# Performance work log

Measured on AMD Instinct MI355X. Metric: run time of the kernel, lower is better.

## Reference

```python
import jax, jax.numpy as jnp
import numpy as np

N = 100000
E = 1600000
F_IN = 32
HID = 16


def _sage_conv(x, src, dst, W_l, b_l, W_r):
    # PyG SAGEConv (aggr='mean', normalize=False, root_weight=True):
    #   out = lin_l(mean_{j in N(i)} x_j) + lin_r(x_i)
    # lin_l has bias, lin_r has no bias.
    n = x.shape[0]
    msg_sum = jax.ops.segment_sum(x[src], dst, num_segments=n)          # [N, d]
    deg = jax.ops.segment_sum(jnp.ones_like(dst, dtype=x.dtype), dst, num_segments=n)
    agg = msg_sum / jnp.maximum(deg, 1.0)[:, None]                      # mean, 0 for isolated nodes
    return agg @ W_l.T + b_l + x @ W_r.T


def setup_inputs() -> dict:
    key = jax.random.key(0)
    ks = jax.random.split(key, 8)
    x = jax.random.normal(ks[0], (N, F_IN), dtype=jnp.float32)
    edge_index = jax.random.randint(ks[1], (1, 2, E), 0, N, dtype=jnp.int64)
    s1 = 1.0 / np.sqrt(F_IN)
    s2 = 1.0 / np.sqrt(HID)
    W1_l = jax.random.uniform(ks[2], (HID, F_IN), jnp.float32, -s1, s1)
    b1_l = jax.random.uniform(ks[3], (HID,), jnp.float32, -s1, s1)
    W1_r = jax.random.uniform(ks[4], (HID, F_IN), jnp.float32, -s1, s1)
    W2_l = jax.random.uniform(ks[5], (F_IN, HID), jnp.float32, -s2, s2)
    b2_l = jax.random.uniform(ks[6], (F_IN,), jnp.float32, -s2, s2)
    W2_r = jax.random.uniform(ks[7], (F_IN, HID), jnp.float32, -s2, s2)
    return {"x": x, "edge_index": edge_index, "W1_l": W1_l, "b1_l": b1_l,
            "W1_r": W1_r, "W2_l": W2_l, "b2_l": b2_l, "W2_r": W2_r}


def reference(x, edge_index, W1_l, b1_l, W1_r, W2_l, b2_l, W2_r):
    ei = jnp.squeeze(edge_index, axis=0)  # [2, E]
    src, dst = ei[0], ei[1]
    h = jax.nn.relu(_sage_conv(x, src, dst, W1_l, b1_l, W1_r))
    out = _sage_conv(h, src, dst, W2_l, b2_l, W2_r)
    return out
```

## Files before the change

kernel.cpp:

```cpp
#include <hip/hip_runtime.h>

#define F_IN 32
#define HID 16
#define BSHIFT 7
#define BNODES (1 << BSHIFT)
#define CAP 2560
#define CHUNK 8192
#define SRCM 0x1FFFFu
#define WS1 33
#define WS2 17

__device__ __forceinline__ void add4(float4& a, const float4& b) {
    a.x += b.x; a.y += b.y; a.z += b.z; a.w += b.w;
}
__device__ __forceinline__ unsigned pack2(float a, float b) {
    unsigned ua = __float_as_uint(a);
    unsigned ub = __float_as_uint(b);
    ua = (ua + 0x7FFFu + ((ua >> 16) & 1u)) >> 16;
    ub = (ub + 0x7FFFu + ((ub >> 16) & 1u)) >> 16;
    return ua | (ub << 16);
}
__device__ __forceinline__ float lo2f(unsigned u) { return __uint_as_float(u << 16); }
__device__ __forceinline__ float hi2f(unsigned u) { return __uint_as_float(u & 0xFFFF0000u); }
__device__ __forceinline__ float4 unp(uint2 v) {
    return make_float4(lo2f(v.x), hi2f(v.x), lo2f(v.y), hi2f(v.y));
}

__global__ void __launch_bounds__(256) k_pre(const float* __restrict__ x,
                                             const float* __restrict__ W1_l,
                                             unsigned* __restrict__ y1b,
                                             const int* __restrict__ ei,
                                             int* __restrict__ bucketCursor,
                                             unsigned* __restrict__ bucketBuf,
                                             int N, int E, int nodeBlocks) {
    __shared__ int cnt[1024];
    __shared__ int runBase[1024];
    __shared__ float Ws[HID * F_IN];
    int tid = threadIdx.x;

    if ((int)blockIdx.x < nodeBlocks) {
        for (int i = tid; i < HID * F_IN; i += 256) Ws[i] = W1_l[i];
        __syncthreads();
        int node = blockIdx.x * 256 + tid;
        if (node >= N) return;
        float xr[F_IN];
        const float4* xp = (const float4*)(x + (size_t)node * F_IN);
#pragma unroll
        for (int i = 0; i < F_IN / 4; i++) {
            float4 v = xp[i];
            xr[4 * i + 0] = v.x; xr[4 * i + 1] = v.y;
            xr[4 * i + 2] = v.z; xr[4 * i + 3] = v.w;
        }
        float a[HID];
#pragma unroll
        for (int o = 0; o < HID; o++) {
            float s = 0.f;
#pragma unroll
            for (int k = 0; k < F_IN; k++) s += xr[k] * Ws[o * F_IN + k];
            a[o] = s;
        }
        uint4* yp = (uint4*)(y1b + (size_t)node * 8);
        yp[0] = make_uint4(pack2(a[0], a[1]), pack2(a[2], a[3]),
                           pack2(a[4], a[5]), pack2(a[6], a[7]));
        yp[1] = make_uint4(pack2(a[8], a[9]), pack2(a[10], a[11]),
                           pack2(a[12], a[13]), pack2(a[14], a[15]));
        return;
    }

    int pb = blockIdx.x - nodeBlocks;
    int e0 = pb * CHUNK;
    int e1 = min(e0 + CHUNK, E);
    int n4 = (e1 - e0) >> 2;
    const int4* dst4 = (const int4*)(ei + E + e0);
    const int4* src4 = (const int4*)(ei + e0);

#pragma unroll
    for (int i = 0; i < 4; i++) cnt[tid + 256 * i] = 0;
    __syncthreads();
    for (int i = tid; i < n4; i += 256) {
        int4 d = dst4[i];
        atomicAdd(&cnt[d.x >> BSHIFT], 1);
        atomicAdd(&cnt[d.y >> BSHIFT], 1);
        atomicAdd(&cnt[d.z >> BSHIFT], 1);
        atomicAdd(&cnt[d.w >> BSHIFT], 1);
    }
    __syncthreads();
#pragma unroll
    for (int i = 0; i < 4; i++) {
        int b = tid + 256 * i;
        int c = cnt[b];
        runBase[b] = c ? atomicAdd(&bucketCursor[b], c) : 0;
        cnt[b] = 0;
    }
    __syncthreads();
    for (int i = tid; i < n4; i += 256) {
        int4 d = dst4[i];
        int4 s = src4[i];
        {
            int b = d.x >> BSHIFT;
            int pos = runBase[b] + atomicAdd(&cnt[b], 1);
            if (pos < CAP)
                bucketBuf[(size_t)b * CAP + pos] = ((unsigned)(d.x & (BNODES - 1)) << 17) | (unsigned)s.x;
        }
        {
            int b = d.y >> BSHIFT;
            int pos = runBase[b] + atomicAdd(&cnt[b], 1);
            if (pos < CAP)
                bucketBuf[(size_t)b * CAP + pos] = ((unsigned)(d.y & (BNODES - 1)) << 17) | (unsigned)s.y;
        }
        {
            int b = d.z >> BSHIFT;
            int pos = runBase[b] + atomicAdd(&cnt[b], 1);
            if (pos < CAP)
                bucketBuf[(size_t)b * CAP + pos] = ((unsigned)(d.z & (BNODES - 1)) << 17) | (unsigned)s.z;
        }
        {
            int b = d.w >> BSHIFT;
            int pos = runBase[b] + atomicAdd(&cnt[b], 1);
            if (pos < CAP)
                bucketBuf[(size_t)b * CAP + pos] = ((unsigned)(d.w & (BNODES - 1)) << 17) | (unsigned)s.w;
        }
    }
}

__global__ void __launch_bounds__(256) k_agg1f(const unsigned* __restrict__ y1b,
                                               const float* __restrict__ x,
                                               unsigned* __restrict__ bucketBuf,
                                               const int* __restrict__ bucketCursor,
                                               const float* __restrict__ W1_r,
                                               const float* __restrict__ b1,
                                               unsigned* __restrict__ hb,
                                               int* __restrict__ meta, int N) {
    __shared__ __align__(16) unsigned sA[CAP];
    __shared__ __align__(16) unsigned sB[CAP];
    __shared__ int hist[BNODES];
    __shared__ int scn[BNODES];
    __shared__ int cur[BNODES];
    __shared__ float Ws[HID * WS1];
    __shared__ float bs[HID];
    int tid = threadIdx.x, b = blockIdx.x;

    for (int i = tid; i < HID * F_IN; i += 256) Ws[(i >> 5) * WS1 + (i & 31)] = W1_r[i];
    if (tid < HID) bs[tid] = b1[tid];
    if (tid < BNODES) hist[tid] = 0;
    int nRec = min(bucketCursor[b], CAP);
    unsigned* buf = bucketBuf + (size_t)b * CAP;
    int n4s = (nRec + 3) >> 2;
    for (int i = tid; i < n4s; i += 256)
        ((uint4*)sA)[i] = ((const uint4*)buf)[i];
    __syncthreads();
    for (int i = tid; i < nRec; i += 256) atomicAdd(&hist[sA[i] >> 17], 1);
    __syncthreads();
    if (tid < BNODES) scn[tid] = hist[tid];
    __syncthreads();
    for (int off = 1; off < BNODES; off <<= 1) {
        int v = (tid < BNODES && tid >= off) ? scn[tid - off] : 0;
        __syncthreads();
        if (tid < BNODES && tid >= off) scn[tid] += v;
        __syncthreads();
    }
    if (tid < BNODES) cur[tid] = scn[tid] - hist[tid];
    __syncthreads();
    for (int i = tid; i < nRec; i += 256) {
        unsigned r = sA[i];
        int pos = atomicAdd(&cur[r >> 17], 1);
        sB[pos] = r & SRCM;
    }
    __syncthreads();

    for (int i = tid; i < n4s; i += 256)
        ((uint4*)buf)[i] = ((const uint4*)sB)[i];
    if (tid < BNODES) {
        meta[(size_t)b * 256 + tid] = scn[tid] - hist[tid];
        meta[(size_t)b * 256 + BNODES + tid] = scn[tid];
    }

    const uint2* yv = (const uint2*)y1b;
#pragma unroll
    for (int pass = 0; pass < 2; pass++) {
        int slot = pass * 256 + tid;
        int nl = slot >> 2, c = slot & 3;
        int node = b * BNODES + nl;
        if (node >= N) continue;
        int start = scn[nl] - hist[nl];
        int dg = hist[nl];
        int jend = start + dg;
        float4 a0 = make_float4(0, 0, 0, 0), a1 = a0;
        int j = start;
        for (; j + 4 <= jend; j += 4) {
            unsigned s0 = sB[j], s1 = sB[j + 1], s2 = sB[j + 2], s3 = sB[j + 3];
            uint2 v0 = yv[(size_t)s0 * 4 + c];
            uint2 v1 = yv[(size_t)s1 * 4 + c];
            uint2 v2 = yv[(size_t)s2 * 4 + c];
            uint2 v3 = yv[(size_t)s3 * 4 + c];
            add4(a0, unp(v0)); add4(a1, unp(v1));
            add4(a0, unp(v2)); add4(a1, unp(v3));
        }
        for (; j < jend; j++) {
            uint2 v = yv[(size_t)sB[j] * 4 + c];
            add4(a0, unp(v));
        }
        add4(a0, a1);
        float inv = 1.0f / (float)(dg > 0 ? dg : 1);
        float m[4] = {a0.x * inv, a0.y * inv, a0.z * inv, a0.w * inv};

        float xr[F_IN];
        const float4* xp = (const float4*)(x + (size_t)node * F_IN);
#pragma unroll
        for (int q = 0; q < F_IN / 4; q++) {
            float4 v = xp[q];
            xr[4 * q + 0] = v.x; xr[4 * q + 1] = v.y;
            xr[4 * q + 2] = v.z; xr[4 * q + 3] = v.w;
        }
        float a[4];
#pragma unroll
        for (int jj = 0; jj < 4; jj++) {
            int o = c * 4 + jj;
            float s = m[jj] + bs[o];
#pragma unroll
            for (int k = 0; k < F_IN; k++) s += xr[k] * Ws[o * WS1 + k];
            a[jj] = fmaxf(s, 0.0f);
        }
        ((uint2*)hb)[(size_t)node * 4 + c] = make_uint2(pack2(a[0], a[1]), pack2(a[2], a[3]));
    }
}

__global__ void __launch_bounds__(256) k_l2f(const unsigned* __restrict__ hb,
                                             const unsigned* __restrict__ bucketBuf,
                                             const int* __restrict__ bucketCursor,
                                             const int* __restrict__ meta,
                                             const float* __restrict__ W2_l,
                                             const float* __restrict__ b2,
                                             const float* __restrict__ W2_r,
                                             float* __restrict__ out, int N) {
    __shared__ __align__(16) unsigned sB[CAP];
    __shared__ int s0[BNODES];
    __shared__ int s1[BNODES];
    __shared__ float mm[BNODES * (HID + 1)];
    __shared__ float Wl[F_IN * WS2];
    __shared__ float Wr[F_IN * WS2];
    __shared__ float bs[F_IN];
    int tid = threadIdx.x, b = blockIdx.x;

    for (int i = tid; i < F_IN * HID; i += 256) {
        int r = i >> 4, q = i & 15;
        Wl[r * WS2 + q] = W2_l[i];
        Wr[r * WS2 + q] = W2_r[i];
    }
    if (tid < F_IN) bs[tid] = b2[tid];
    if (tid < BNODES) {
        s0[tid] = meta[(size_t)b * 256 + tid];
        s1[tid] = meta[(size_t)b * 256 + BNODES + tid];
    }
    int nRec = min(bucketCursor[b], CAP);
    const uint4* bv = (const uint4*)(bucketBuf + (size_t)b * CAP);
    int n4s = (nRec + 3) >> 2;
    for (int i = tid; i < n4s; i += 256) ((uint4*)sB)[i] = bv[i];
    __syncthreads();

    const uint2* hv = (const uint2*)hb;
#pragma unroll
    for (int pass = 0; pass < 2; pass++) {
        int slot = pass * 256 + tid;
        int nl = slot >> 2, c = slot & 3;
        int node = b * BNODES + nl;
        if (node >= N) continue;
        int start = s0[nl];
        int jend = s1[nl];
        int dg = jend - start;
        float4 a0 = make_float4(0, 0, 0, 0), a1 = a0;
        int j = start;
        for (; j + 4 <= jend; j += 4) {
            unsigned v0i = sB[j], v1i = sB[j + 1], v2i = sB[j + 2], v3i = sB[j + 3];
            uint2 v0 = hv[(size_t)v0i * 4 + c];
            uint2 v1 = hv[(size_t)v1i * 4 + c];
            uint2 v2 = hv[(size_t)v2i * 4 + c];
            uint2 v3 = hv[(size_t)v3i * 4 + c];
            add4(a0, unp(v0)); add4(a1, unp(v1));
            add4(a0, unp(v2)); add4(a1, unp(v3));
        }
        for (; j < jend; j++) {
            uint2 v = hv[(size_t)sB[j] * 4 + c];
            add4(a0, unp(v));
        }
        add4(a0, a1);
        float inv = 1.0f / (float)(dg > 0 ? dg : 1);
        mm[nl * (HID + 1) + c * 4 + 0] = a0.x * inv;
        mm[nl * (HID + 1) + c * 4 + 1] = a0.y * inv;
        mm[nl * (HID + 1) + c * 4 + 2] = a0.z * inv;
        mm[nl * (HID + 1) + c * 4 + 3] = a0.w * inv;
    }
    __syncthreads();

#pragma unroll
    for (int pass = 0; pass < 2; pass++) {
        int slot = pass * 256 + tid;
        int nl = slot >> 2, c = slot & 3;
        int node = b * BNODES + nl;
        if (node >= N) continue;

        float m[HID];
#pragma unroll
        for (int k = 0; k < HID; k++) m[k] = mm[nl * (HID + 1) + k];

        float hr[HID];
        const uint4* hp = (const uint4*)(hb + (size_t)node * 8);
        uint4 u0 = hp[0], u1 = hp[1];
        hr[0] = lo2f(u0.x); hr[1] = hi2f(u0.x); hr[2] = lo2f(u0.y); hr[3] = hi2f(u0.y);
        hr[4] = lo2f(u0.z); hr[5] = hi2f(u0.z); hr[6] = lo2f(u0.w); hr[7] = hi2f(u0.w);
        hr[8] = lo2f(u1.x); hr[9] = hi2f(u1.x); hr[10] = lo2f(u1.y); hr[11] = hi2f(u1.y);
        hr[12] = lo2f(u1.z); hr[13] = hi2f(u1.z); hr[14] = lo2f(u1.w); hr[15] = hi2f(u1.w);

        float a[8];
#pragma unroll
        for (int jj = 0; jj < 8; jj++) {
            int o = c * 8 + jj;
            float s = bs[o];
#pragma unroll
            for (int k = 0; k < HID; k++)
                s += m[k] * Wl[o * WS2 + k] + hr[k] * Wr[o * WS2 + k];
            a[jj] = s;
        }
        float4* op = (float4*)(out + (size_t)node * F_IN + c * 8);
        op[0] = make_float4(a[0], a[1], a[2], a[3]);
        op[1] = make_float4(a[4], a[5], a[6], a[7]);
    }
}

extern "C" void kernel_launch(void* const* d_in, const int* in_sizes, int n_in,
                              void* d_out, int out_size, void* d_ws, size_t ws_size,
                              hipStream_t stream) {
    const float* x    = (const float*)d_in[0];
    const int*   ei   = (const int*)d_in[1];
    const float* W1_l = (const float*)d_in[2];
    const float* b1   = (const float*)d_in[3];
    const float* W1_r = (const float*)d_in[4];
    const float* W2_l = (const float*)d_in[5];
    const float* b2   = (const float*)d_in[6];
    const float* W2_r = (const float*)d_in[7];
    float* out = (float*)d_out;

    const int N = in_sizes[0] / F_IN;
    const int E = in_sizes[1] / 2;
    const int nbuckets = (N + BNODES - 1) >> BSHIFT;

    int* bucketCursor = (int*)d_ws;
    unsigned* bucketBuf = (unsigned*)(bucketCursor + 1024);
    unsigned* y1b = bucketBuf + (size_t)nbuckets * CAP;
    unsigned* hb  = y1b + (size_t)N * 8;
    int* meta = (int*)(hb + (size_t)N * 8);

    hipMemsetAsync(bucketCursor, 0, 1024 * sizeof(int), stream);

    const int nodeBlocks = (N + 255) / 256;
    const int partBlocks = (E + CHUNK - 1) / CHUNK;

    k_pre<<<nodeBlocks + partBlocks, 256, 0, stream>>>(x, W1_l, y1b, ei,
                                                       bucketCursor, bucketBuf,
                                                       N, E, nodeBlocks);
    k_agg1f<<<nbuckets, 256, 0, stream>>>(y1b, x, bucketBuf, bucketCursor,
                                          W1_r, b1, hb, meta, N);
    k_l2f<<<nbuckets, 256, 0, stream>>>(hb, bucketBuf, bucketCursor, meta,
                                        W2_l, b2, W2_r, out, N);
}
```

Before: 152.0 us.

## Locally sort edge chunks in LDS and precompute root transform in pre-kernel

The edge partition blocks now counting-sort their chunk by bucket in shared memory first, then write each bucket's records to global memory as contiguous runs. This replaces the scattered per-edge global writes and is meant to improve write coalescing. The chunk size is halved so the sorted chunk fits in shared memory. The layer-1 root projection (x·W1_r plus bias) also moves into the node blocks of the pre-kernel and is stored as an fp32 buffer, so the aggregation kernel no longer rereads x or does the matmul. The cost is an extra 64 bytes per node of global traffic and more partition blocks with a scan step.

After: 172.8 us. 1.14x slower.

```diff
diff --git a/kernel.cpp b/kernel.cpp
--- a/kernel.cpp
+++ b/kernel.cpp
@@ -5,9 +5,9 @@
 #define BSHIFT 7
 #define BNODES (1 << BSHIFT)
 #define CAP 2560
-#define CHUNK 8192
+#define CHUNK 4096
+#define NBINS 1024
 #define SRCM 0x1FFFFu
-#define WS1 33
 #define WS2 17
 
 __device__ __forceinline__ void add4(float4& a, const float4& b) {
@@ -28,18 +28,23 @@
 
 __global__ void __launch_bounds__(256) k_pre(const float* __restrict__ x,
                                              const float* __restrict__ W1_l,
+                                             const float* __restrict__ b1,
+                                             const float* __restrict__ W1_r,
                                              unsigned* __restrict__ y1b,
+                                             float* __restrict__ y1r,
                                              const int* __restrict__ ei,
                                              int* __restrict__ bucketCursor,
                                              unsigned* __restrict__ bucketBuf,
                                              int N, int E, int nodeBlocks) {
-    __shared__ int cnt[1024];
-    __shared__ int runBase[1024];
-    __shared__ float Ws[HID * F_IN];
+    __shared__ __align__(16) unsigned char smem[37888];
     int tid = threadIdx.x;
 
     if ((int)blockIdx.x < nodeBlocks) {
-        for (int i = tid; i < HID * F_IN; i += 256) Ws[i] = W1_l[i];
+        float* Wa = (float*)smem;
+        float* Wb = (float*)(smem + 2048);
+        float* bb = (float*)(smem + 4096);
+        for (int i = tid; i < HID * F_IN; i += 256) { Wa[i] = W1_l[i]; Wb[i] = W1_r[i]; }
+        if (tid < HID) bb[tid] = b1[tid];
         __syncthreads();
         int node = blockIdx.x * 256 + tid;
         if (node >= N) return;
@@ -56,7 +61,7 @@
         for (int o = 0; o < HID; o++) {
             float s = 0.f;
 #pragma unroll
-            for (int k = 0; k < F_IN; k++) s += xr[k] * Ws[o * F_IN + k];
+            for (int k = 0; k < F_IN; k++) s += xr[k] * Wa[o * F_IN + k];
             a[o] = s;
         }
         uint4* yp = (uint4*)(y1b + (size_t)node * 8);
@@ -64,71 +69,108 @@
                            pack2(a[4], a[5]), pack2(a[6], a[7]));
         yp[1] = make_uint4(pack2(a[8], a[9]), pack2(a[10], a[11]),
                            pack2(a[12], a[13]), pack2(a[14], a[15]));
+#pragma unroll
+        for (int o = 0; o < HID; o++) {
+            float s = bb[o];
+#pragma unroll
+            for (int k = 0; k < F_IN; k++) s += xr[k] * Wb[o * F_IN + k];
+            a[o] = s;
+        }
+        float4* rp = (float4*)(y1r + (size_t)node * HID);
+        rp[0] = make_float4(a[0], a[1], a[2], a[3]);
+        rp[1] = make_float4(a[4], a[5], a[6], a[7]);
+        rp[2] = make_float4(a[8], a[9], a[10], a[11]);
+        rp[3] = make_float4(a[12], a[13], a[14], a[15]);
         return;
     }
+
+    unsigned* sRec = (unsigned*)smem;
+    unsigned short* sBkt = (unsigned short*)(smem + 16384);
+    int* hist    = (int*)(smem + 24576);
+    int* cur     = (int*)(smem + 28672);
+    int* runBase = (int*)(smem + 32768);
+    int* tmp     = (int*)(smem + 36864);
 
     int pb = blockIdx.x - nodeBlocks;
     int e0 = pb * CHUNK;
-    int e1 = min(e0 + CHUNK, E);
-    int n4 = (e1 - e0) >> 2;
+    int n = min(CHUNK, E - e0);
+    int n4 = n >> 2;
     const int4* dst4 = (const int4*)(ei + E + e0);
     const int4* src4 = (const int4*)(ei + e0);
 
 #pragma unroll
-    for (int i = 0; i < 4; i++) cnt[tid + 256 * i] = 0;
+    for (int i = 0; i < 4; i++) hist[tid + 256 * i] = 0;
     __syncthreads();
     for (int i = tid; i < n4; i += 256) {
         int4 d = dst4[i];
-        atomicAdd(&cnt[d.x >> BSHIFT], 1);
-        atomicAdd(&cnt[d.y >> BSHIFT], 1);
-        atomicAdd(&cnt[d.z >> BSHIFT], 1);
-        atomicAdd(&cnt[d.w >> BSHIFT], 1);
-    }
-    __syncthreads();
-#pragma unroll
-    for (int i = 0; i < 4; i++) {
-        int b = tid + 256 * i;
-        int c = cnt[b];
-        runBase[b] = c ? atomicAdd(&bucketCursor[b], c) : 0;
-        cnt[b] = 0;
-    }
+        atomicAdd(&hist[d.x >> BSHIFT], 1);
+        atomicAdd(&hist[d.y >> BSHIFT], 1);
+        atomicAdd(&hist[d.z >> BSHIFT], 1);
+        atomicAdd(&hist[d.w >> BSHIFT], 1);
+    }
+    __syncthreads();
+    int h0 = hist[4 * tid + 0], h1 = hist[4 * tid + 1];
+    int h2 = hist[4 * tid + 2], h3 = hist[4 * tid + 3];
+    int ssum = h0 + h1 + h2 + h3;
+    tmp[tid] = ssum;
+    __syncthreads();
+    for (int off = 1; off < 256; off <<= 1) {
+        int v = (tid >= off) ? tmp[tid - off] : 0;
+        __syncthreads();
+        if (tid >= off) tmp[tid] += v;
+        __syncthreads();
+    }
+    int excl = tmp[tid] - ssum;
+    cur[4 * tid + 0] = excl;
+    cur[4 * tid + 1] = excl + h0;
+    cur[4 * tid + 2] = excl + h0 + h1;
+    cur[4 * tid + 3] = excl + h0 + h1 + h2;
+    runBase[4 * tid + 0] = h0 ? atomicAdd(&bucketCursor[4 * tid + 0], h0) : 0;
+    runBase[4 * tid + 1] = h1 ? atomicAdd(&bucketCursor[4 * tid + 1], h1) : 0;
+    runBase[4 * tid + 2] = h2 ? atomicAdd(&bucketCursor[4 * tid + 2], h2) : 0;
+    runBase[4 * tid + 3] = h3 ? atomicAdd(&bucketCursor[4 * tid + 3], h3) : 0;
     __syncthreads();
     for (int i = tid; i < n4; i += 256) {
         int4 d = dst4[i];
         int4 s = src4[i];
         {
             int b = d.x >> BSHIFT;
-            int pos = runBase[b] + atomicAdd(&cnt[b], 1);
-            if (pos < CAP)
-                bucketBuf[(size_t)b * CAP + pos] = ((unsigned)(d.x & (BNODES - 1)) << 17) | (unsigned)s.x;
+            int pos = atomicAdd(&cur[b], 1);
+            sRec[pos] = ((unsigned)(d.x & (BNODES - 1)) << 17) | (unsigned)s.x;
+            sBkt[pos] = (unsigned short)b;
         }
         {
             int b = d.y >> BSHIFT;
-            int pos = runBase[b] + atomicAdd(&cnt[b], 1);
-            if (pos < CAP)
-                bucketBuf[(size_t)b * CAP + pos] = ((unsigned)(d.y & (BNODES - 1)) << 17) | (unsigned)s.y;
+            int pos = atomicAdd(&cur[b], 1);
+            sRec[pos] = ((unsigned)(d.y & (BNODES - 1)) << 17) | (unsigned)s.y;
+            sBkt[pos] = (unsigned short)b;
         }
         {
             int b = d.z >> BSHIFT;
-            int pos = runBase[b] + atomicAdd(&cnt[b], 1);
-            if (pos < CAP)
-                bucketBuf[(size_t)b * CAP + pos] = ((unsigned)(d.z & (BNODES - 1)) << 17) | (unsigned)s.z;
+            int pos = atomicAdd(&cur[b], 1);
+            sRec[pos] = ((unsigned)(d.z & (BNODES - 1)) << 17) | (unsigned)s.z;
+            sBkt[pos] = (unsigned short)b;
         }
         {
             int b = d.w >> BSHIFT;
-            int pos = runBase[b] + atomicAdd(&cnt[b], 1);
-            if (pos < CAP)
-                bucketBuf[(size_t)b * CAP + pos] = ((unsigned)(d.w & (BNODES - 1)) << 17) | (unsigned)s.w;
-        }
+            int pos = atomicAdd(&cur[b], 1);
+            sRec[pos] = ((unsigned)(d.w & (BNODES - 1)) << 17) | (unsigned)s.w;
+            sBkt[pos] = (unsigned short)b;
+        }
+    }
+    __syncthreads();
+    for (int p = tid; p < n; p += 256) {
+        int b = sBkt[p];
+        int start = cur[b] - hist[b];
+        int bpos = runBase[b] + (p - start);
+        if (bpos < CAP) bucketBuf[(size_t)b * CAP + bpos] = sRec[p];
     }
 }
 
 __global__ void __launch_bounds__(256) k_agg1f(const unsigned* __restrict__ y1b,
-                                               const float* __restrict__ x,
+                                               const float* __restrict__ y1r,
                                                unsigned* __restrict__ bucketBuf,
                                                const int* __restrict__ bucketCursor,
-                                               const float* __restrict__ W1_r,
-                                               const float* __restrict__ b1,
                                                unsigned* __restrict__ hb,
                                                int* __restrict__ meta, int N) {
     __shared__ __align__(16) unsigned sA[CAP];
@@ -136,12 +178,8 @@
     __shared__ int hist[BNODES];
     __shared__ int scn[BNODES];
     __shared__ int cur[BNODES];
-    __shared__ float Ws[HID * WS1];
-    __shared__ float bs[HID];
     int tid = threadIdx.x, b = blockIdx.x;
 
-    for (int i = tid; i < HID * F_IN; i += 256) Ws[(i >> 5) * WS1 + (i & 31)] = W1_r[i];
-    if (tid < HID) bs[tid] = b1[tid];
     if (tid < BNODES) hist[tid] = 0;
     int nRec = min(bucketCursor[b], CAP);
     unsigned* buf = bucketBuf + (size_t)b * CAP;
@@ -202,26 +240,12 @@
         }
         add4(a0, a1);
         float inv = 1.0f / (float)(dg > 0 ? dg : 1);
-        float m[4] = {a0.x * inv, a0.y * inv, a0.z * inv, a0.w * inv};
-
-        float xr[F_IN];
-        const float4* xp = (const float4*)(x + (size_t)node * F_IN);
-#pragma unroll
-        for (int q = 0; q < F_IN / 4; q++) {
-            float4 v = xp[q];
-            xr[4 * q + 0] = v.x; xr[4 * q + 1] = v.y;
-            xr[4 * q + 2] = v.z; xr[4 * q + 3] = v.w;
-        }
-        float a[4];
-#pragma unroll
-        for (int jj = 0; jj < 4; jj++) {
-            int o = c * 4 + jj;
-            float s = m[jj] + bs[o];
-#pragma unroll
-            for (int k = 0; k < F_IN; k++) s += xr[k] * Ws[o * WS1 + k];
-            a[jj] = fmaxf(s, 0.0f);
-        }
-        ((uint2*)hb)[(size_t)node * 4 + c] = make_uint2(pack2(a[0], a[1]), pack2(a[2], a[3]));
+        float4 r4 = ((const float4*)(y1r + (size_t)node * HID))[c];
+        float o0 = fmaxf(a0.x * inv + r4.x, 0.0f);
+        float o1 = fmaxf(a0.y * inv + r4.y, 0.0f);
+        float o2 = fmaxf(a0.z * inv + r4.z, 0.0f);
+        float o3 = fmaxf(a0.w * inv + r4.w, 0.0f);
+        ((uint2*)hb)[(size_t)node * 4 + c] = make_uint2(pack2(o0, o1), pack2(o2, o3));
     }
 }
 
@@ -349,17 +373,19 @@
     unsigned* y1b = bucketBuf + (size_t)nbuckets * CAP;
     unsigned* hb  = y1b + (size_t)N * 8;
     int* meta = (int*)(hb + (size_t)N * 8);
+    float* y1r = (float*)(meta + (size_t)nbuckets * 256);
 
     hipMemsetAsync(bucketCursor, 0, 1024 * sizeof(int), stream);
 
     const int nodeBlocks = (N + 255) / 256;
     const int partBlocks = (E + CHUNK - 1) / CHUNK;
 
-    k_pre<<<nodeBlocks + partBlocks, 256, 0, stream>>>(x, W1_l, y1b, ei,
+    k_pre<<<nodeBlocks + partBlocks, 256, 0, stream>>>(x, W1_l, b1, W1_r,
+                                                       y1b, y1r, ei,
                                                        bucketCursor, bucketBuf,
                                                        N, E, nodeBlocks);
-    k_agg1f<<<nbuckets, 256, 0, stream>>>(y1b, x, bucketBuf, bucketCursor,
-                                          W1_r, b1, hb, meta, N);
+    k_agg1f<<<nbuckets, 256, 0, stream>>>(y1b, y1r, bucketBuf, bucketCursor,
+                                          hb, meta, N);
     k_l2f<<<nbuckets, 256, 0, stream>>>(hb, bucketBuf, bucketCursor, meta,
                                         W2_l, b2, W2_r, out, N);
 }
```

## Halve bucket size and move root linear transform into precompute kernel

Applied to the files above, without the earlier changes.

Buckets now hold 64 destination nodes instead of 128, which doubles the number of aggregation blocks (about 1563 per kernel) and gives each thread a single node-chunk slot instead of two passes. The x @ W1_r + b1 root term moves from the layer-1 aggregation kernel to the node blocks of the precompute kernel and is stored as an fp32 buffer, so the aggregation kernel only adds it after the mean. This is meant to raise parallelism and cut per-block work and shared memory in the aggregation kernels. The cost is a larger partition histogram (2048 bins), an extra 6.4 MB fp32 write and read, and a per-bucket capacity of 1440 with little headroom above the mean of about 1024 edges per bucket.

Measured after the change: 147.3 us (median of 2 runs). 3.1% less time.

```diff
diff --git a/kernel.cpp b/kernel.cpp
--- a/kernel.cpp
+++ b/kernel.cpp
@@ -2,12 +2,12 @@
 
 #define F_IN 32
 #define HID 16
-#define BSHIFT 7
+#define BSHIFT 6
 #define BNODES (1 << BSHIFT)
-#define CAP 2560
+#define CAP 1440
+#define NBINS 2048
 #define CHUNK 8192
 #define SRCM 0x1FFFFu
-#define WS1 33
 #define WS2 17
 
 __device__ __forceinline__ void add4(float4& a, const float4& b) {
@@ -28,18 +28,24 @@
 
 __global__ void __launch_bounds__(256) k_pre(const float* __restrict__ x,
                                              const float* __restrict__ W1_l,
+                                             const float* __restrict__ b1,
+                                             const float* __restrict__ W1_r,
                                              unsigned* __restrict__ y1b,
+                                             float* __restrict__ y1r,
                                              const int* __restrict__ ei,
                                              int* __restrict__ bucketCursor,
                                              unsigned* __restrict__ bucketBuf,
                                              int N, int E, int nodeBlocks) {
-    __shared__ int cnt[1024];
-    __shared__ int runBase[1024];
-    __shared__ float Ws[HID * F_IN];
+    __shared__ int cnt[NBINS];
+    __shared__ int runBase[NBINS];
+    __shared__ float Wa[HID * F_IN];
+    __shared__ float Wb[HID * F_IN];
+    __shared__ float bb[HID];
     int tid = threadIdx.x;
 
     if ((int)blockIdx.x < nodeBlocks) {
-        for (int i = tid; i < HID * F_IN; i += 256) Ws[i] = W1_l[i];
+        for (int i = tid; i < HID * F_IN; i += 256) { Wa[i] = W1_l[i]; Wb[i] = W1_r[i]; }
+        if (tid < HID) bb[tid] = b1[tid];
         __syncthreads();
         int node = blockIdx.x * 256 + tid;
         if (node >= N) return;
@@ -56,7 +62,7 @@
         for (int o = 0; o < HID; o++) {
             float s = 0.f;
 #pragma unroll
-            for (int k = 0; k < F_IN; k++) s += xr[k] * Ws[o * F_IN + k];
+            for (int k = 0; k < F_IN; k++) s += xr[k] * Wa[o * F_IN + k];
             a[o] = s;
         }
         uint4* yp = (uint4*)(y1b + (size_t)node * 8);
@@ -64,6 +70,18 @@
                            pack2(a[4], a[5]), pack2(a[6], a[7]));
         yp[1] = make_uint4(pack2(a[8], a[9]), pack2(a[10], a[11]),
                            pack2(a[12], a[13]), pack2(a[14], a[15]));
+#pragma unroll
+        for (int o = 0; o < HID; o++) {
+            float s = bb[o];
+#pragma unroll
+            for (int k = 0; k < F_IN; k++) s += xr[k] * Wb[o * F_IN + k];
+            a[o] = s;
+        }
+        float4* rp = (float4*)(y1r + (size_t)node * HID);
+        rp[0] = make_float4(a[0], a[1], a[2], a[3]);
+        rp[1] = make_float4(a[4], a[5], a[6], a[7]);
+        rp[2] = make_float4(a[8], a[9], a[10], a[11]);
+        rp[3] = make_float4(a[12], a[13], a[14], a[15]);
         return;
     }
 
@@ -75,7 +93,7 @@
     const int4* src4 = (const int4*)(ei + e0);
 
 #pragma unroll
-    for (int i = 0; i < 4; i++) cnt[tid + 256 * i] = 0;
+    for (int i = 0; i < NBINS / 256; i++) cnt[tid + 256 * i] = 0;
     __syncthreads();
     for (int i = tid; i < n4; i += 256) {
         int4 d = dst4[i];
@@ -86,7 +104,7 @@
     }
     __syncthreads();
 #pragma unroll
-    for (int i = 0; i < 4; i++) {
+    for (int i = 0; i < NBINS / 256; i++) {
         int b = tid + 256 * i;
         int c = cnt[b];
         runBase[b] = c ? atomicAdd(&bucketCursor[b], c) : 0;
@@ -124,11 +142,9 @@
 }
 
 __global__ void __launch_bounds__(256) k_agg1f(const unsigned* __restrict__ y1b,
-                                               const float* __restrict__ x,
+                                               const float* __restrict__ y1r,
                                                unsigned* __restrict__ bucketBuf,
                                                const int* __restrict__ bucketCursor,
-                                               const float* __restrict__ W1_r,
-                                               const float* __restrict__ b1,
                                                unsigned* __restrict__ hb,
                                                int* __restrict__ meta, int N) {
     __shared__ __align__(16) unsigned sA[CAP];
@@ -136,12 +152,8 @@
     __shared__ int hist[BNODES];
     __shared__ int scn[BNODES];
     __shared__ int cur[BNODES];
-    __shared__ float Ws[HID * WS1];
-    __shared__ float bs[HID];
     int tid = threadIdx.x, b = blockIdx.x;
 
-    for (int i = tid; i < HID * F_IN; i += 256) Ws[(i >> 5) * WS1 + (i & 31)] = W1_r[i];
-    if (tid < HID) bs[tid] = b1[tid];
     if (tid < BNODES) hist[tid] = 0;
     int nRec = min(bucketCursor[b], CAP);
     unsigned* buf = bucketBuf + (size_t)b * CAP;
@@ -171,57 +183,42 @@
     for (int i = tid; i < n4s; i += 256)
         ((uint4*)buf)[i] = ((const uint4*)sB)[i];
     if (tid < BNODES) {
-        meta[(size_t)b * 256 + tid] = scn[tid] - hist[tid];
-        meta[(size_t)b * 256 + BNODES + tid] = scn[tid];
+        meta[(size_t)b * 128 + tid] = scn[tid] - hist[tid];
+        meta[(size_t)b * 128 + BNODES + tid] = scn[tid];
     }
 
     const uint2* yv = (const uint2*)y1b;
-#pragma unroll
-    for (int pass = 0; pass < 2; pass++) {
-        int slot = pass * 256 + tid;
-        int nl = slot >> 2, c = slot & 3;
+    {
+        int nl = tid >> 2, c = tid & 3;
         int node = b * BNODES + nl;
-        if (node >= N) continue;
-        int start = scn[nl] - hist[nl];
-        int dg = hist[nl];
-        int jend = start + dg;
-        float4 a0 = make_float4(0, 0, 0, 0), a1 = a0;
-        int j = start;
-        for (; j + 4 <= jend; j += 4) {
-            unsigned s0 = sB[j], s1 = sB[j + 1], s2 = sB[j + 2], s3 = sB[j + 3];
-            uint2 v0 = yv[(size_t)s0 * 4 + c];
-            uint2 v1 = yv[(size_t)s1 * 4 + c];
-            uint2 v2 = yv[(size_t)s2 * 4 + c];
-            uint2 v3 = yv[(size_t)s3 * 4 + c];
-            add4(a0, unp(v0)); add4(a1, unp(v1));
-            add4(a0, unp(v2)); add4(a1, unp(v3));
-        }
-        for (; j < jend; j++) {
-            uint2 v = yv[(size_t)sB[j] * 4 + c];
-            add4(a0, unp(v));
-        }
-        add4(a0, a1);
-        float inv = 1.0f / (float)(dg > 0 ? dg : 1);
-        float m[4] = {a0.x * inv, a0.y * inv, a0.z * inv, a0.w * inv};
-
-        float xr[F_IN];
-        const float4* xp = (const float4*)(x + (size_t)node * F_IN);
-#pragma unroll
-        for (int q = 0; q < F_IN / 4; q++) {
-            float4 v = xp[q];
-            xr[4 * q + 0] = v.x; xr[4 * q + 1] = v.y;
-            xr[4 * q + 2] = v.z; xr[4 * q + 3] = v.w;
-        }
-        float a[4];
-#pragma unroll
-        for (int jj = 0; jj < 4; jj++) {
-            int o = c * 4 + jj;
-            float s = m[jj] + bs[o];
-#pragma unroll
-            for (int k = 0; k < F_IN; k++) s += xr[k] * Ws[o * WS1 + k];
-            a[jj] = fmaxf(s, 0.0f);
-        }
-        ((uint2*)hb)[(size_t)node * 4 + c] = make_uint2(pack2(a[0], a[1]), pack2(a[2], a[3]));
+        if (node < N) {
+            int start = scn[nl] - hist[nl];
+            int dg = hist[nl];
+            int jend = start + dg;
+            float4 a0 = make_float4(0, 0, 0, 0), a1 = a0;
+            int j = start;
+            for (; j + 4 <= jend; j += 4) {
+                unsigned s0 = sB[j], s1 = sB[j + 1], s2 = sB[j + 2], s3 = sB[j + 3];
+                uint2 v0 = yv[(size_t)s0 * 4 + c];
+                uint2 v1 = yv[(size_t)s1 * 4 + c];
+                uint2 v2 = yv[(size_t)s2 * 4 + c];
+                uint2 v3 = yv[(size_t)s3 * 4 + c];
+                add4(a0, unp(v0)); add4(a1, unp(v1));
+                add4(a0, unp(v2)); add4(a1, unp(v3));
+            }
+            for (; j < jend; j++) {
+                uint2 v = yv[(size_t)sB[j] * 4 + c];
+                add4(a0, unp(v));
+            }
+            add4(a0, a1);
+            float inv = 1.0f / (float)(dg > 0 ? dg : 1);
+            float4 r4 = ((const float4*)(y1r + (size_t)node * HID))[c];
+            float o0 = fmaxf(a0.x * inv + r4.x, 0.0f);
+            float o1 = fmaxf(a0.y * inv + r4.y, 0.0f);
+            float o2 = fmaxf(a0.z * inv + r4.z, 0.0f);
+            float o3 = fmaxf(a0.w * inv + r4.w, 0.0f);
+            ((uint2*)hb)[(size_t)node * 4 + c] = make_uint2(pack2(o0, o1), pack2(o2, o3));
+        }
     }
 }
 
@@ -249,8 +246,8 @@
     }
     if (tid < F_IN) bs[tid] = b2[tid];
     if (tid < BNODES) {
-        s0[tid] = meta[(size_t)b * 256 + tid];
-        s1[tid] = meta[(size_t)b * 256 + BNODES + tid];
+        s0[tid] = meta[(size_t)b * 128 + tid];
+        s1[tid] = meta[(size_t)b * 128 + BNODES + tid];
     }
     int nRec = min(bucketCursor[b], CAP);
     const uint4* bv = (const uint4*)(bucketBuf + (size_t)b * CAP);
@@ -259,45 +256,42 @@
     __syncthreads();
 
     const uint2* hv = (const uint2*)hb;
-#pragma unroll
-    for (int pass = 0; pass < 2; pass++) {
-        int slot = pass * 256 + tid;
-        int nl = slot >> 2, c = slot & 3;
+    {
+        int nl = tid >> 2, c = tid & 3;
         int node = b * BNODES + nl;
-        if (node >= N) continue;
-        int start = s0[nl];
-        int jend = s1[nl];
-        int dg = jend - start;
-        float4 a0 = make_float4(0, 0, 0, 0), a1 = a0;
-        int j = start;
-        for (; j + 4 <= jend; j += 4) {
-            unsigned v0i = sB[j], v1i = sB[j + 1], v2i = sB[j + 2], v3i = sB[j + 3];
-            uint2 v0 = hv[(size_t)v0i * 4 + c];
-            uint2 v1 = hv[(size_t)v1i * 4 + c];
-            uint2 v2 = hv[(size_t)v2i * 4 + c];
-            uint2 v3 = hv[(size_t)v3i * 4 + c];
-            add4(a0, unp(v0)); add4(a1, unp(v1));
-            add4(a0, unp(v2)); add4(a1, unp(v3));
-        }
-        for (; j < jend; j++) {
-            uint2 v = hv[(size_t)sB[j] * 4 + c];
-            add4(a0, unp(v));
-        }
-        add4(a0, a1);
-        float inv = 1.0f / (float)(dg > 0 ? dg : 1);
-        mm[nl * (HID + 1) + c * 4 + 0] = a0.x * inv;
-        mm[nl * (HID + 1) + c * 4 + 1] = a0.y * inv;
-        mm[nl * (HID + 1) + c * 4 + 2] = a0.z * inv;
-        mm[nl * (HID + 1) + c * 4 + 3] = a0.w * inv;
-    }
-    __syncthreads();
-
-#pragma unroll
-    for (int pass = 0; pass < 2; pass++) {
-        int slot = pass * 256 + tid;
-        int nl = slot >> 2, c = slot & 3;
+        if (node < N) {
+            int start = s0[nl];
+            int jend = s1[nl];
+            int dg = jend - start;
+            float4 a0 = make_float4(0, 0, 0, 0), a1 = a0;
+            int j = start;
+            for (; j + 4 <= jend; j += 4) {
+                unsigned v0i = sB[j], v1i = sB[j + 1], v2i = sB[j + 2], v3i = sB[j + 3];
+                uint2 v0 = hv[(size_t)v0i * 4 + c];
+                uint2 v1 = hv[(size_t)v1i * 4 + c];
+                uint2 v2 = hv[(size_t)v2i * 4 + c];
+                uint2 v3 = hv[(size_t)v3i * 4 + c];
+                add4(a0, unp(v0)); add4(a1, unp(v1));
+                add4(a0, unp(v2)); add4(a1, unp(v3));
+            }
+            for (; j < jend; j++) {
+                uint2 v = hv[(size_t)sB[j] * 4 + c];
+                add4(a0, unp(v));
+            }
+            add4(a0, a1);
+            float inv = 1.0f / (float)(dg > 0 ? dg : 1);
+            mm[nl * (HID + 1) + c * 4 + 0] = a0.x * inv;
+            mm[nl * (HID + 1) + c * 4 + 1] = a0.y * inv;
+            mm[nl * (HID + 1) + c * 4 + 2] = a0.z * inv;
+            mm[nl * (HID + 1) + c * 4 + 3] = a0.w * inv;
+        }
+    }
+    __syncthreads();
+
+    {
+        int nl = tid >> 2, c = tid & 3;
         int node = b * BNODES + nl;
-        if (node >= N) continue;
+        if (node >= N) return;
 
         float m[HID];
 #pragma unroll
@@ -345,21 +339,23 @@
     const int nbuckets = (N + BNODES - 1) >> BSHIFT;
 
     int* bucketCursor = (int*)d_ws;
-    unsigned* bucketBuf = (unsigned*)(bucketCursor + 1024);
+    unsigned* bucketBuf = (unsigned*)(bucketCursor + NBINS);
     unsigned* y1b = bucketBuf + (size_t)nbuckets * CAP;
     unsigned* hb  = y1b + (size_t)N * 8;
     int* meta = (int*)(hb + (size_t)N * 8);
-
-    hipMemsetAsync(bucketCursor, 0, 1024 * sizeof(int), stream);
+    float* y1r = (float*)(meta + (size_t)nbuckets * 128);
+
+    hipMemsetAsync(bucketCursor, 0, NBINS * sizeof(int), stream);
 
     const int nodeBlocks = (N + 255) / 256;
     const int partBlocks = (E + CHUNK - 1) / CHUNK;
 
-    k_pre<<<nodeBlocks + partBlocks, 256, 0, stream>>>(x, W1_l, y1b, ei,
+    k_pre<<<nodeBlocks + partBlocks, 256, 0, stream>>>(x, W1_l, b1, W1_r,
+                                                       y1b, y1r, ei,
                                                        bucketCursor, bucketBuf,
                                                        N, E, nodeBlocks);
-    k_agg1f<<<nbuckets, 256, 0, stream>>>(y1b, x, bucketBuf, bucketCursor,
-                                          W1_r, b1, hb, meta, N);
+    k_agg1f<<<nbuckets, 256, 0, stream>>>(y1b, y1r, bucketBuf, bucketCursor,
+                                          hb, meta, N);
     k_l2f<<<nbuckets, 256, 0, stream>>>(hb, bucketBuf, bucketCursor, meta,
                                         W2_l, b2, W2_r, out, N);
 }
```
